# Optimization experiments

Hardware: AMD Instinct MI355X
Metric: run time of the kernel (lower is better)

The kernel has to match this reference:

```python
import jax, jax.numpy as jnp
import numpy as np

N, T, F_IN, HID, LAT, E = 20000, 16, 65, 128, 64, 320000
F = F_IN - 1


def setup_inputs() -> dict:
    key = jax.random.key(0)
    ks = jax.random.split(key, 10)
    def w(k, shape, fan):
        return jax.random.normal(k, shape, jnp.float32) / np.sqrt(fan).astype(np.float32)
    return dict(
        x=jax.random.normal(ks[0], (N, T, F_IN), jnp.float32),
        enc_W=w(ks[1], (F, HID), F), enc_b=jnp.zeros((HID,), jnp.float32),
        enc_ln_g=jnp.ones((HID,), jnp.float32), enc_ln_b=jnp.zeros((HID,), jnp.float32),
        lstm1_Wih=w(ks[2], (HID, 4 * LAT), HID), lstm1_Whh=w(ks[3], (LAT, 4 * LAT), LAT),
        lstm1_b=jnp.zeros((4 * LAT,), jnp.float32),
        lstm2_Wih=w(ks[4], (LAT, 4 * HID), LAT), lstm2_Whh=w(ks[5], (HID, 4 * HID), HID),
        lstm2_b=jnp.zeros((4 * HID,), jnp.float32),
        dec_ln_g=jnp.ones((HID,), jnp.float32), dec_ln_b=jnp.zeros((HID,), jnp.float32),
        dec_W=w(ks[6], (HID, F), HID), dec_b=jnp.zeros((F,), jnp.float32),
        edge_index=jax.random.randint(ks[7], (2, E), 0, N, dtype=jnp.int64),
    )


def _ln(x, g, b):
    m = x.mean(-1, keepdims=True)
    v = x.var(-1, keepdims=True)
    return (x - m) * jax.lax.rsqrt(v + 1e-5) * g + b


def _gcn(xs, W, b, src, dst, dinv):
    # xs: (T, N, Fin); PyG GCNConv: sym-normalized A+I, then linear. Linear first (same math).
    n = xs.shape[1]
    xw = jnp.einsum('tnf,fh->tnh', xs, W)
    norm = (dinv[src] * dinv[dst])[:, None]  # (E,1)
    def body(_, xt):  # scatter one frame at a time to bound (E,H) intermediate
        return None, jax.ops.segment_sum(xt[src] * norm, dst, num_segments=n)
    _, agg = jax.lax.scan(body, None, xw)
    # self-loop term: norm_ii = dinv_i^2
    return agg + (dinv ** 2)[None, :, None] * xw + b


def _lstm(x_seq, Wih, Whh, b):
    # x_seq: (S, B, in) -> outputs (S, B, H); PyTorch gate order i,f,g,o
    H = Whh.shape[0]
    B = x_seq.shape[1]
    def step(carry, xt):
        h, c = carry
        gates = xt @ Wih + h @ Whh + b
        i, f, g, o = jnp.split(gates, 4, axis=-1)
        c = jax.nn.sigmoid(f) * c + jax.nn.sigmoid(i) * jnp.tanh(g)
        h = jax.nn.sigmoid(o) * jnp.tanh(c)
        return (h, c), h
    z0 = jnp.zeros((B, H), x_seq.dtype)
    _, hs = jax.lax.scan(step, (z0, z0), x_seq)
    return hs


def reference(x, enc_W, enc_b, enc_ln_g, enc_ln_b,
              lstm1_Wih, lstm1_Whh, lstm1_b,
              lstm2_Wih, lstm2_Whh, lstm2_b,
              dec_ln_g, dec_ln_b, dec_W, dec_b, edge_index):
    src, dst = edge_index[0], edge_index[1]
    deg = jax.ops.segment_sum(jnp.ones(src.shape[0], x.dtype), dst,
                              num_segments=x.shape[0]) + 1.0  # +1 for self loop
    dinv = jax.lax.rsqrt(deg)
    importance = x[:, :, -1:]                      # (N,T,1)
    xs = (x[:, :, :-1] * importance).transpose(1, 0, 2)   # frame-major (T,N,F)
    h = _ln(_gcn(xs, enc_W, enc_b, src, dst, dinv), enc_ln_g, enc_ln_b)  # (T,N,HID)
    # temporal encoder: batch=N nodes, sequence over T frames
    z = _lstm(h, lstm1_Wih, lstm1_Whh, lstm1_b)    # (T,N,LAT)
    z_nt = z.transpose(1, 0, 2)                    # (N,T,LAT)
    # temporal decoder: original code feeds (1, N, LAT) per frame -> sequence over
    # NODES with fresh state each frame; batch the T independent frames together.
    hd = _lstm(z_nt, lstm2_Wih, lstm2_Whh, lstm2_b)  # scan over nodes -> (N,T,HID)
    hd = _ln(hd.transpose(1, 0, 2), dec_ln_g, dec_ln_b)  # (T,N,HID)
    rec = _gcn(hd, dec_W, dec_b, src, dst, dinv).transpose(1, 0, 2)  # (N,T,F)
    reconstructed = jnp.concatenate([rec, importance], axis=2)        # (N,T,F_IN)
    return z_nt, reconstructed
```

## Files before the change

### kernel.cpp

```cpp
#include <hip/hip_runtime.h>
#include <hip/hip_fp16.h>
#include <stdint.h>

#define N_NODES 20000
#define T_STEPS 16
#define F_INPUT 65
#define F_DIM   64
#define HID     128
#define LAT     64
#define N_EDGES 320000

#define WARMUP  32

typedef _Float16 f16x8 __attribute__((ext_vector_type(8)));
typedef float f32x4 __attribute__((ext_vector_type(4)));

__device__ __forceinline__ float rcp_fast(float x){ return __builtin_amdgcn_rcpf(x); }
__device__ __forceinline__ float sigm(float x){ return rcp_fast(1.0f + __expf(-x)); }
__device__ __forceinline__ float tanh_fast(float x){
  float e = __expf(2.0f * x);
  return 1.0f - 2.0f * rcp_fast(e + 1.0f);
}

__global__ void k_zero(int* deg){
  int i = blockIdx.x * 256 + threadIdx.x;
  if (i < N_NODES) deg[i] = 0;
}

__global__ void k_count(const int* __restrict__ ei, int* __restrict__ deg){
  int e = blockIdx.x * 256 + threadIdx.x;
  if (e < N_EDGES) atomicAdd(&deg[ei[N_EDGES + e]], 1);
}

__global__ void k_scan(const int* __restrict__ deg, int* __restrict__ offs,
                       float* __restrict__ dinv, int* __restrict__ cursor){
  __shared__ int sbuf[1024];
  __shared__ int carry;
  int tid = threadIdx.x;
  if (tid == 0){ carry = 0; offs[0] = 0; }
  __syncthreads();
  for (int base = 0; base < N_NODES; base += 1024){
    int cb = carry;
    int v = (base + tid < N_NODES) ? deg[base + tid] : 0;
    sbuf[tid] = v;
    __syncthreads();
    for (int off = 1; off < 1024; off <<= 1){
      int add = (tid >= off) ? sbuf[tid - off] : 0;
      __syncthreads();
      sbuf[tid] += add;
      __syncthreads();
    }
    if (base + tid < N_NODES){
      offs[base + tid + 1] = cb + sbuf[tid];
      cursor[base + tid] = cb + sbuf[tid] - v;
      dinv[base + tid] = rsqrtf((float)v + 1.0f);
    }
    __syncthreads();
    if (tid == 1023) carry = cb + sbuf[1023];
    __syncthreads();
  }
}

__global__ void k_fill(const int* __restrict__ ei, const float* __restrict__ dinv,
                       int* __restrict__ cursor, int* __restrict__ csrc,
                       float* __restrict__ cw){
  int e = blockIdx.x * 256 + threadIdx.x;
  if (e < N_EDGES){
    int s = ei[e], d = ei[N_EDGES + e];
    int p = atomicAdd(&cursor[d], 1);
    csrc[p] = s;
    cw[p] = dinv[s] * dinv[d];
  }
}

__global__ void k_xsw(const float* __restrict__ x, __half* __restrict__ xsw){
  int idx = blockIdx.x * 256 + threadIdx.x;
  if (idx < N_NODES * T_STEPS * F_DIM){
    int nt = idx >> 6;
    int k = idx & 63;
    float imp = x[(size_t)nt * F_INPUT + F_DIM];
    xsw[idx] = __float2half(x[(size_t)nt * F_INPUT + k] * imp);
  }
}

__device__ __forceinline__ void acc_row(uint2 rv, float wv,
                                        float& a0, float& a1, float& a2, float& a3){
  __half2 h01 = __builtin_bit_cast(__half2, rv.x);
  __half2 h23 = __builtin_bit_cast(__half2, rv.y);
  a0 += wv * __half2float(h01.x); a1 += wv * __half2float(h01.y);
  a2 += wv * __half2float(h23.x); a3 += wv * __half2float(h23.y);
}

__global__ void k_wprep(const float* __restrict__ W1ih, const float* __restrict__ W1hh,
                        const float* __restrict__ Wih2, const float* __restrict__ Whh2,
                        const float* __restrict__ encW, const float* __restrict__ decW,
                        __half* __restrict__ WB1, __half* __restrict__ WZ2,
                        __half* __restrict__ WB2, __half* __restrict__ WBe,
                        __half* __restrict__ WBd){
  int idx = blockIdx.x * 256 + threadIdx.x;
  if (idx < 49152){
    int j = idx & 7;
    int lane = (idx >> 3) & 63;
    int tk = idx >> 9;
    int kt = tk % 6;
    int T = tk / 6;
    int k = 32 * kt + 8 * (lane >> 4) + j;
    int col = 16 * T + (lane & 15);
    float v = (k < 128) ? W1ih[k * 256 + col] : W1hh[(k - 128) * 256 + col];
    WB1[idx] = __float2half(v);
  } else if (idx < 81920){
    int i2 = idx - 49152;
    int j = i2 & 7;
    int lane = (i2 >> 3) & 63;
    int fid = i2 >> 9;
    int kt = fid & 1;
    int T = fid >> 1;
    int k = 32 * kt + 8 * (lane >> 4) + j;
    int col = 16 * T + (lane & 15);
    WZ2[i2] = __float2half(Wih2[k * 512 + col]);
  } else if (idx < 147456){
    int i2 = idx - 81920;
    int j = i2 & 7;
    int lane = (i2 >> 3) & 63;
    int kt = (i2 >> 9) & 3;
    int T = i2 >> 11;
    int k = 32 * kt + 8 * (lane >> 4) + j;
    int col = T * 16 + (lane & 15);
    WB2[i2] = __float2half(Whh2[k * 512 + col]);
  } else if (idx < 155648){
    int i2 = idx - 147456;
    int j = i2 & 7;
    int lane = (i2 >> 3) & 63;
    int fid = i2 >> 9;
    int kt = fid & 1;
    int T = fid >> 1;
    int k = 32 * kt + 8 * (lane >> 4) + j;
    int col = 16 * T + (lane & 15);
    WBe[i2] = __float2half(encW[k * 128 + col]);
  } else if (idx < 163840){
    int i2 = idx - 155648;
    int j = i2 & 7;
    int lane = (i2 >> 3) & 63;
    int fid = i2 >> 9;
    int kt = fid & 3;
    int T = fid >> 2;
    int k = 32 * kt + 8 * (lane >> 4) + j;
    int col = 16 * T + (lane & 15);
    WBd[i2] = __float2half(decW[k * 64 + col]);
  }
}

__global__ __launch_bounds__(256) void k_enc(
    const __half* __restrict__ xsw, const int* __restrict__ offs,
    const int* __restrict__ csrc, const float* __restrict__ cw,
    const float* __restrict__ dinv, const __half* __restrict__ WBe,
    const float* __restrict__ encb, const float* __restrict__ lng,
    const float* __restrict__ lnb, __half* __restrict__ henc){
  __shared__ __align__(16) char ush[16 * 160];
  __shared__ float hb[16 * 132];
  const int tid = threadIdx.x;
  const int w = tid >> 6, lane = tid & 63;
  const int qf = lane & 15, gf = lane >> 4;
  const int t = tid >> 4, q = tid & 15;
  const f32x4 z4 = {0.f, 0.f, 0.f, 0.f};

  f16x8 wbe[2][2];
  float eb[2];
  {
    const f16x8* Bp = (const f16x8*)WBe;
    #pragma unroll
    for (int tt = 0; tt < 2; ++tt){
      #pragma unroll
      for (int kt = 0; kt < 2; ++kt)
        wbe[tt][kt] = Bp[((2 * w + tt) * 2 + kt) * 64 + lane];
      eb[tt] = encb[16 * (2 * w + tt) + qf];
    }
  }

  for (int nn = 0; nn < 4; ++nn){
    int n = blockIdx.x * 4 + nn;
    __syncthreads();
    float a0 = 0.f, a1 = 0.f, a2 = 0.f, a3 = 0.f;
    int beg = offs[n], end = offs[n + 1];
    int e = beg;
    for (; e + 8 <= end; e += 8){
      int sx[8]; float wx[8]; uint2 rx[8];
      #pragma unroll
      for (int k = 0; k < 8; ++k){ sx[k] = csrc[e + k]; wx[k] = cw[e + k]; }
      #pragma unroll
      for (int k = 0; k < 8; ++k)
        rx[k] = *reinterpret_cast<const uint2*>(&xsw[((size_t)(sx[k] * 16 + t)) * 64 + 4 * q]);
      #pragma unroll
      for (int k = 0; k < 8; ++k) acc_row(rx[k], wx[k], a0, a1, a2, a3);
    }
    for (; e < end; ++e){
      int s = csrc[e];
      float wv = cw[e];
      uint2 rv = *reinterpret_cast<const uint2*>(&xsw[((size_t)(s * 16 + t)) * 64 + 4 * q]);
      acc_row(rv, wv, a0, a1, a2, a3);
    }
    float di = dinv[n];
    float d2 = di * di;
    {
      uint2 rv = *reinterpret_cast<const uint2*>(&xsw[((size_t)(n * 16 + t)) * 64 + 4 * q]);
      acc_row(rv, d2, a0, a1, a2, a3);
    }
    {
      __half2 p01 = __floats2half2_rn(a0, a1);
      __half2 p23 = __floats2half2_rn(a2, a3);
      uint2 pk;
      pk.x = __builtin_bit_cast(uint32_t, p01);
      pk.y = __builtin_bit_cast(uint32_t, p23);
      *(uint2*)(ush + t * 160 + 8 * q) = pk;
    }
    __syncthreads();
    {
      f16x8 A0 = *(const f16x8*)(ush + qf * 160 + 16 * gf);
      f16x8 A1 = *(const f16x8*)(ush + qf * 160 + 64 + 16 * gf);
      #pragma unroll
      for (int tt = 0; tt < 2; ++tt){
        f32x4 acc = __builtin_amdgcn_mfma_f32_16x16x32_f16(A0, wbe[tt][0], z4, 0, 0, 0);
        acc = __builtin_amdgcn_mfma_f32_16x16x32_f16(A1, wbe[tt][1], acc, 0, 0, 0);
        #pragma unroll
        for (int r = 0; r < 4; ++r)
          hb[(4 * gf + r) * 132 + 16 * (2 * w + tt) + qf] = acc[r] + eb[tt];
      }
    }
    __syncthreads();
    {
      float v[8];
      float s1 = 0.f, s2 = 0.f;
      #pragma unroll
      for (int r = 0; r < 8; ++r){
        v[r] = hb[t * 132 + q + 16 * r];
        s1 += v[r]; s2 += v[r] * v[r];
      }
      #pragma unroll
      for (int m = 1; m < 16; m <<= 1){
        s1 += __shfl_xor(s1, m, 16);
        s2 += __shfl_xor(s2, m, 16);
      }
      float mean = s1 * (1.0f / 128.0f);
      float var = s2 * (1.0f / 128.0f) - mean * mean;
      float rstd = rsqrtf(var + 1e-5f);
      #pragma unroll
      for (int r = 0; r < 8; ++r){
        int j = q + 16 * r;
        henc[((size_t)t * N_NODES + n) * 128 + j] =
            __float2half((v[r] - mean) * rstd * lng[j] + lnb[j]);
      }
    }
  }
}

__global__ __launch_bounds__(256) void k_l1mm(
    const __half* __restrict__ henc, const __half* __restrict__ WB1,
    const float* __restrict__ b1, float* __restrict__ out0,
    __half* __restrict__ zh){
  __shared__ __align__(16) char xt[16 * 272];
  __shared__ __align__(16) char hs[2][16 * 144];
  const int tid = threadIdx.x;
  const int w = tid >> 6, lane = tid & 63;
  const int q = lane & 15, g = lane >> 4;
  const int n0 = blockIdx.x * 16;
  const int u = 16 * w + q;
  const f32x4 z4 = {0.f, 0.f, 0.f, 0.f};

  f16x8 wb[4][6];
  {
    const f16x8* WBp = (const f16x8*)WB1;
    #pragma unroll
    for (int gate = 0; gate < 4; ++gate){
      #pragma unroll
      for (int kt = 0; kt < 6; ++kt){
        wb[gate][kt] = WBp[((4 * gate + w) * 6 + kt) * 64 + lane];
      }
    }
  }
  float bi = b1[u], bf = b1[64 + u], bg = b1[128 + u], bo = b1[192 + u];

  for (int i = tid; i < 576; i += 256) *(int*)(hs[0] + 4 * i) = 0;
  float creg[4] = {0.f, 0.f, 0.f, 0.f};
  const int sni = tid >> 4, sk0 = (tid & 15) * 8;
  const __half* hsrc0 = henc + ((size_t)(n0 + sni) * 128 + sk0);

  #pragma unroll 1
  for (int t = 0; t < T_STEPS; ++t){
    __syncthreads();
    *(f16x8*)(xt + sni * 272 + 2 * sk0) = *(const f16x8*)(hsrc0 + (size_t)t * N_NODES * 128);
    __syncthreads();
    const char* hrow = hs[t & 1] + q * 144 + 16 * g;
    f16x8 a0 = *(const f16x8*)(xt + 272 * q + 16 * g);
    f16x8 a1 = *(const f16x8*)(xt + 272 * q + 64 + 16 * g);
    f16x8 a2 = *(const f16x8*)(xt + 272 * q + 128 + 16 * g);
    f16x8 a3 = *(const f16x8*)(xt + 272 * q + 192 + 16 * g);
    f16x8 a4 = *(const f16x8*)(hrow);
    f16x8 a5 = *(const f16x8*)(hrow + 64);
    f32x4 ai = z4, af = z4, ag = z4, ao = z4;
#define MF(A, B, C) __builtin_amdgcn_mfma_f32_16x16x32_f16((A), (B), (C), 0, 0, 0)
    ai = MF(a0, wb[0][0], ai); af = MF(a0, wb[1][0], af);
    ag = MF(a0, wb[2][0], ag); ao = MF(a0, wb[3][0], ao);
    ai = MF(a1, wb[0][1], ai); af = MF(a1, wb[1][1], af);
    ag = MF(a1, wb[2][1], ag); ao = MF(a1, wb[3][1], ao);
    ai = MF(a2, wb[0][2], ai); af = MF(a2, wb[1][2], af);
    ag = MF(a2, wb[2][2], ag); ao = MF(a2, wb[3][2], ao);
    ai = MF(a3, wb[0][3], ai); af = MF(a3, wb[1][3], af);
    ag = MF(a3, wb[2][3], ag); ao = MF(a3, wb[3][3], ao);
    ai = MF(a4, wb[0][4], ai); af = MF(a4, wb[1][4], af);
    ag = MF(a4, wb[2][4], ag); ao = MF(a4, wb[3][4], ao);
    ai = MF(a5, wb[0][5], ai); af = MF(a5, wb[1][5], af);
    ag = MF(a5, wb[2][5], ag); ao = MF(a5, wb[3][5], ao);
#undef MF
    #pragma unroll
    for (int r = 0; r < 4; ++r){
      int node = 4 * g + r;
      float gi = ai[r] + bi, gf = af[r] + bf;
      float gg = ag[r] + bg, go = ao[r] + bo;
      float c = sigm(gf) * creg[r] + sigm(gi) * tanh_fast(gg);
      creg[r] = c;
      float h = sigm(go) * tanh_fast(c);
      _Float16 hh = (_Float16)h;
      *(_Float16*)(hs[(t + 1) & 1] + node * 144 + 2 * u) = hh;
      size_t oidx = ((size_t)(n0 + node) * 16 + t) * 64 + u;
      out0[oidx] = h;
      zh[oidx] = __builtin_bit_cast(__half, hh);
    }
  }
}

__global__ __launch_bounds__(512) void k_lstm2(
    const __half* __restrict__ zh, const __half* __restrict__ WB2,
    const __half* __restrict__ WZ2, const float* __restrict__ b2,
    __half* __restrict__ hd){
  __shared__ __align__(16) char hls[2][16 * 288];
  const int tid = threadIdx.x;
  const int w = tid >> 6;
  const int lane = tid & 63;
  const int q = lane & 15;
  const int g = lane >> 4;
  const int s = blockIdx.x;
  const int u = 16 * w + q;
  const int n0 = 78 * s + (s < 32 ? s : 32);
  const int n1 = n0 + (s < 32 ? 79 : 78);
  const int n_start = (s == 0) ? 0 : (n0 - WARMUP);
  const f32x4 zz4 = {0.f, 0.f, 0.f, 0.f};

  f16x8 wb[4][4];
  f16x8 wz[4][2];
  {
    const f16x8* WBp = (const f16x8*)WB2;
    const f16x8* WZp = (const f16x8*)WZ2;
    #pragma unroll
    for (int gate = 0; gate < 4; ++gate){
      #pragma unroll
      for (int kt = 0; kt < 4; ++kt)
        wb[gate][kt] = WBp[((gate * 8 + w) * 4 + kt) * 64 + lane];
      #pragma unroll
      for (int kt = 0; kt < 2; ++kt)
        wz[gate][kt] = WZp[((gate * 8 + w) * 2 + kt) * 64 + lane];
    }
  }
  const float b_i = b2[128 * 0 + u];
  const float b_f = b2[128 * 1 + u];
  const float b_g = b2[128 * 2 + u];
  const float b_o = b2[128 * 3 + u];

  for (int i = tid; i < 2304; i += 512) ((int*)hls)[i] = 0;

  int rdoff[4];
  #pragma unroll
  for (int kt = 0; kt < 4; ++kt)
    rdoff[kt] = q * 288 + 64 * kt + 16 * g;

  const __half* zq = zh + 64 * q + 8 * g;
  f16x8 za0k0, za0k1, za1k0, za1k1, za2k0, za2k1, za3k0, za3k1;
#define LDZ(K0, K1, NN)                                                        \
  { const __half* p_ = zq + (size_t)(NN) * 1024;                               \
    K0 = *(const f16x8*)(p_); K1 = *(const f16x8*)(p_ + 32); }
  LDZ(za0k0, za0k1, n_start + 0)
  LDZ(za1k0, za1k1, n_start + 1)
  LDZ(za2k0, za2k1, n_start + 2)
  LDZ(za3k0, za3k1, n_start + 3)

  float creg[4] = {0.f, 0.f, 0.f, 0.f};
  __half* hdp = hd + u;
  __syncthreads();

#define MFM(A, B, C) __builtin_amdgcn_mfma_f32_16x16x32_f16((A), (B), (C), 0, 0, 0)
#define L2_CORE(CUR, ZK0, ZK1, DO_STORE, NN)                                   \
  {                                                                            \
    const char* rb = hls[CUR];                                                 \
    f16x8 a0 = *(const f16x8*)(rb + rdoff[0]);                                 \
    f16x8 a1 = *(const f16x8*)(rb + rdoff[1]);                                 \
    f16x8 a2 = *(const f16x8*)(rb + rdoff[2]);                                 \
    f16x8 a3 = *(const f16x8*)(rb + rdoff[3]);                                 \
    f32x4 acc[4];                                                              \
    _Pragma("unroll")                                                          \
    for (int gate = 0; gate < 4; ++gate){                                      \
      acc[gate] = MFM(ZK0, wz[gate][0], zz4);                                  \
      acc[gate] = MFM(ZK1, wz[gate][1], acc[gate]);                            \
    }                                                                          \
    _Pragma("unroll")                                                          \
    for (int gate = 0; gate < 4; ++gate) acc[gate] = MFM(a0, wb[gate][0], acc[gate]); \
    _Pragma("unroll")                                                          \
    for (int gate = 0; gate < 4; ++gate) acc[gate] = MFM(a1, wb[gate][1], acc[gate]); \
    _Pragma("unroll")                                                          \
    for (int gate = 0; gate < 4; ++gate) acc[gate] = MFM(a2, wb[gate][2], acc[gate]); \
    _Pragma("unroll")                                                          \
    for (int gate = 0; gate < 4; ++gate) acc[gate] = MFM(a3, wb[gate][3], acc[gate]); \
    _Pragma("unroll")                                                          \
    for (int r = 0; r < 4; ++r){                                               \
      float gi = acc[0][r] + b_i;                                              \
      float gf = acc[1][r] + b_f;                                              \
      float gg = acc[2][r] + b_g;                                              \
      float go = acc[3][r] + b_o;                                              \
      float ei = __expf(-gi), ef = __expf(-gf);                                \
      float eg = __expf(2.f * gg), eo = __expf(-go);                           \
      float pi1 = 1.f + ei, pf1 = 1.f + ef, pg1 = eg + 1.f;                    \
      float pig_ = pi1 * pg1;                                                  \
      float num = creg[r] * pig_ + (eg - 1.f) * pf1;                           \
      float c = num * rcp_fast(pf1 * pig_);                                    \
      creg[r] = c;                                                             \
      float ec = __expf(2.f * c);                                              \
      float h = (ec - 1.f) * rcp_fast((1.f + eo) * (ec + 1.f));                \
      *(_Float16*)(hls[CUR ^ 1] + (4 * g + r) * 288 + 2 * u) = (_Float16)h;    \
      if (DO_STORE && (NN) < n1)                                               \
        hdp[(size_t)(NN) * 2048 + (4 * g + r) * 128] = __float2half(h);        \
    }                                                                          \
    __builtin_amdgcn_sched_barrier(0);                                         \
    asm volatile("s_waitcnt lgkmcnt(0)" ::: "memory");                         \
    __builtin_amdgcn_s_barrier();                                              \
    __builtin_amdgcn_sched_barrier(0);                                         \
  }

  #pragma unroll 1
  for (int n = n_start; n < n0; n += 4){
    L2_CORE(0, za0k0, za0k1, 0, n)     LDZ(za0k0, za0k1, n + 4)
    L2_CORE(1, za1k0, za1k1, 0, n)     LDZ(za1k0, za1k1, n + 5)
    L2_CORE(0, za2k0, za2k1, 0, n)     LDZ(za2k0, za2k1, n + 6)
    L2_CORE(1, za3k0, za3k1, 0, n)     LDZ(za3k0, za3k1, n + 7)
  }
  #pragma unroll 1
  for (int n = n0; n < n1; n += 4){
    L2_CORE(0, za0k0, za0k1, 1, n + 0) LDZ(za0k0, za0k1, n + 4)
    L2_CORE(1, za1k0, za1k1, 1, n + 1) LDZ(za1k0, za1k1, n + 5)
    L2_CORE(0, za2k0, za2k1, 1, n + 2) LDZ(za2k0, za2k1, n + 6)
    L2_CORE(1, za3k0, za3k1, 1, n + 3) LDZ(za3k0, za3k1, n + 7)
  }
#undef L2_CORE
#undef MFM
#undef LDZ
}

__global__ __launch_bounds__(256) void k_decproj(
    const __half* __restrict__ hd, const __half* __restrict__ WBd,
    const float* __restrict__ lng, const float* __restrict__ lnb,
    __half* __restrict__ y){
  __shared__ float xr[16 * 132];
  __shared__ __align__(16) char xrh[16 * 288];
  const int tid = threadIdx.x;
  const int w = tid >> 6, lane = tid & 63;
  const int qf = lane & 15, gf = lane >> 4;
  const int t = tid >> 4, q = tid & 15;
  const f32x4 z4 = {0.f, 0.f, 0.f, 0.f};

  f16x8 wbd[4];
  {
    const f16x8* Bp = (const f16x8*)WBd;
    #pragma unroll
    for (int kt = 0; kt < 4; ++kt)
      wbd[kt] = Bp[(w * 4 + kt) * 64 + lane];
  }

  for (int nn = 0; nn < 4; ++nn){
    int n = blockIdx.x * 4 + nn;
    __syncthreads();
    {
      f16x8 hv = *(const f16x8*)(hd + (size_t)n * 2048 + tid * 8);
      int tt2 = tid >> 4, k0 = (tid & 15) * 8;
      #pragma unroll
      for (int jj = 0; jj < 8; ++jj) xr[tt2 * 132 + k0 + jj] = (float)hv[jj];
    }
    __syncthreads();
    {
      float v[8];
      float s1 = 0.f, s2 = 0.f;
      #pragma unroll
      for (int r = 0; r < 8; ++r){
        v[r] = xr[t * 132 + q + 16 * r];
        s1 += v[r]; s2 += v[r] * v[r];
      }
      #pragma unroll
      for (int m = 1; m < 16; m <<= 1){
        s1 += __shfl_xor(s1, m, 16);
        s2 += __shfl_xor(s2, m, 16);
      }
      float mean = s1 * (1.0f / 128.0f);
      float var = s2 * (1.0f / 128.0f) - mean * mean;
      float rstd = rsqrtf(var + 1e-5f);
      #pragma unroll
      for (int r = 0; r < 8; ++r){
        int jj = q + 16 * r;
        *(_Float16*)(xrh + t * 288 + 2 * jj) =
            (_Float16)((v[r] - mean) * rstd * lng[jj] + lnb[jj]);
      }
    }
    __syncthreads();
    {
      f16x8 A0 = *(const f16x8*)(xrh + qf * 288 + 16 * gf);
      f16x8 A1 = *(const f16x8*)(xrh + qf * 288 + 64 + 16 * gf);
      f16x8 A2 = *(const f16x8*)(xrh + qf * 288 + 128 + 16 * gf);
      f16x8 A3 = *(const f16x8*)(xrh + qf * 288 + 192 + 16 * gf);
      f32x4 acc = __builtin_amdgcn_mfma_f32_16x16x32_f16(A0, wbd[0], z4, 0, 0, 0);
      acc = __builtin_amdgcn_mfma_f32_16x16x32_f16(A1, wbd[1], acc, 0, 0, 0);
      acc = __builtin_amdgcn_mfma_f32_16x16x32_f16(A2, wbd[2], acc, 0, 0, 0);
      acc = __builtin_amdgcn_mfma_f32_16x16x32_f16(A3, wbd[3], acc, 0, 0, 0);
      #pragma unroll
      for (int r = 0; r < 4; ++r)
        y[((size_t)n * 16 + 4 * gf + r) * 64 + 16 * w + qf] = __float2half(acc[r]);
    }
  }
}

__global__ __launch_bounds__(256) void k_decagg(
    const __half* __restrict__ y, const int* __restrict__ offs,
    const int* __restrict__ csrc, const float* __restrict__ cw,
    const float* __restrict__ dinv, const float* __restrict__ decb,
    const float* __restrict__ x, float* __restrict__ out1){
  int n = blockIdx.x, tid = threadIdx.x;
  int t = tid >> 4, q = tid & 15;
  float a0 = 0.f, a1 = 0.f, a2 = 0.f, a3 = 0.f;
  int beg = offs[n], end = offs[n + 1];
  int e = beg;
  for (; e + 8 <= end; e += 8){
    int sx[8]; float wx[8]; uint2 rx[8];
    #pragma unroll
    for (int k = 0; k < 8; ++k){ sx[k] = csrc[e + k]; wx[k] = cw[e + k]; }
    #pragma unroll
    for (int k = 0; k < 8; ++k)
      rx[k] = *reinterpret_cast<const uint2*>(&y[((size_t)(sx[k] * 16 + t)) * 64 + 4 * q]);
    #pragma unroll
    for (int k = 0; k < 8; ++k) acc_row(rx[k], wx[k], a0, a1, a2, a3);
  }
  for (; e < end; ++e){
    int s = csrc[e];
    float wv = cw[e];
    uint2 rv = *reinterpret_cast<const uint2*>(&y[((size_t)(s * 16 + t)) * 64 + 4 * q]);
    acc_row(rv, wv, a0, a1, a2, a3);
  }
  float di = dinv[n];
  float d2 = di * di;
  {
    uint2 rv = *reinterpret_cast<const uint2*>(&y[((size_t)(n * 16 + t)) * 64 + 4 * q]);
    acc_row(rv, d2, a0, a1, a2, a3);
  }
  a0 += decb[4 * q + 0]; a1 += decb[4 * q + 1];
  a2 += decb[4 * q + 2]; a3 += decb[4 * q + 3];
  size_t ob = ((size_t)n * 16 + t) * 65;
  out1[ob + 4 * q + 0] = a0;
  out1[ob + 4 * q + 1] = a1;
  out1[ob + 4 * q + 2] = a2;
  out1[ob + 4 * q + 3] = a3;
  if (q == 0) out1[ob + 64] = x[((size_t)n * 16 + t) * 65 + 64];
}

extern "C" void kernel_launch(void* const* d_in, const int* in_sizes, int n_in,
                              void* d_out, int out_size, void* d_ws, size_t ws_size,
                              hipStream_t stream){
  (void)in_sizes; (void)n_in; (void)out_size; (void)ws_size;
  const float* x     = (const float*)d_in[0];
  const float* encW  = (const float*)d_in[1];
  const float* encb  = (const float*)d_in[2];
  const float* encg  = (const float*)d_in[3];
  const float* encbl = (const float*)d_in[4];
  const float* W1ih  = (const float*)d_in[5];
  const float* W1hh  = (const float*)d_in[6];
  const float* b1    = (const float*)d_in[7];
  const float* W2ih  = (const float*)d_in[8];
  const float* W2hh  = (const float*)d_in[9];
  const float* b2    = (const float*)d_in[10];
  const float* dlg   = (const float*)d_in[11];
  const float* dlb   = (const float*)d_in[12];
  const float* decW  = (const float*)d_in[13];
  const float* decb  = (const float*)d_in[14];
  const int*   ei    = (const int*)d_in[15];

  char* w = (char*)d_ws;
  auto alloc = [&](size_t bytes) -> char* {
    char* p = w;
    w += (bytes + 255) & ~(size_t)255;
    return p;
  };
  int*   deg    = (int*)  alloc((size_t)N_NODES * 4);
  float* dinv   = (float*)alloc((size_t)N_NODES * 4);
  int*   offs   = (int*)  alloc((size_t)(N_NODES + 1) * 4);
  int*   cursor = (int*)  alloc((size_t)N_NODES * 4);
  int*   csrc   = (int*)  alloc((size_t)N_EDGES * 4);
  float* cwt    = (float*)alloc((size_t)N_EDGES * 4);
  __half* xsw   = (__half*)alloc((size_t)N_NODES * T_STEPS * 64 * 2);
  __half* henc  = (__half*)alloc((size_t)T_STEPS * N_NODES * 128 * 2);
  __half* hd    = (__half*)alloc((size_t)N_NODES * T_STEPS * 128 * 2);
  __half* yh    = (__half*)alloc((size_t)N_NODES * T_STEPS * 64 * 2);
  __half* zh    = (__half*)alloc((size_t)N_NODES * T_STEPS * 64 * 2 + 32768);
  __half* WB1   = (__half*)alloc((size_t)49152 * 2);
  __half* WZ2   = (__half*)alloc((size_t)32768 * 2);
  __half* WB2   = (__half*)alloc((size_t)65536 * 2);
  __half* WBe   = (__half*)alloc((size_t)8192 * 2);
  __half* WBd   = (__half*)alloc((size_t)8192 * 2);

  float* out0 = (float*)d_out;
  float* out1 = out0 + (size_t)N_NODES * T_STEPS * 64;

  k_zero<<<(N_NODES + 255) / 256, 256, 0, stream>>>(deg);
  k_count<<<(N_EDGES + 255) / 256, 256, 0, stream>>>(ei, deg);
  k_scan<<<1, 1024, 0, stream>>>(deg, offs, dinv, cursor);
  k_fill<<<(N_EDGES + 255) / 256, 256, 0, stream>>>(ei, dinv, cursor, csrc, cwt);
  k_xsw<<<(N_NODES * T_STEPS * 64 + 255) / 256, 256, 0, stream>>>(x, xsw);
  k_wprep<<<640, 256, 0, stream>>>(W1ih, W1hh, W2ih, W2hh, encW, decW,
                                   WB1, WZ2, WB2, WBe, WBd);
  k_enc<<<5000, 256, 0, stream>>>(xsw, offs, csrc, cwt, dinv, WBe, encb, encg, encbl, henc);
  k_l1mm<<<1250, 256, 0, stream>>>(henc, WB1, b1, out0, zh);
  k_lstm2<<<256, 512, 0, stream>>>(zh, WB2, WZ2, b2, hd);
  k_decproj<<<5000, 256, 0, stream>>>(hd, WBd, dlg, dlb, yh);
  k_decagg<<<N_NODES, 256, 0, stream>>>(yh, offs, csrc, cwt, dinv, decb, x, out1);
}
```

Before: 544.0 us.

## Process two nodes per 512-thread block in encoder and decoder aggregation; pad LSTM2 LDS rows

```diff
diff --git a/kernel.cpp b/kernel.cpp
--- a/kernel.cpp
+++ b/kernel.cpp
@@ -150,18 +150,21 @@
   }
 }
 
-__global__ __launch_bounds__(256) void k_enc(
+__global__ __launch_bounds__(512) void k_enc(
     const __half* __restrict__ xsw, const int* __restrict__ offs,
     const int* __restrict__ csrc, const float* __restrict__ cw,
     const float* __restrict__ dinv, const __half* __restrict__ WBe,
     const float* __restrict__ encb, const float* __restrict__ lng,
     const float* __restrict__ lnb, __half* __restrict__ henc){
-  __shared__ __align__(16) char ush[16 * 160];
-  __shared__ float hb[16 * 132];
+  __shared__ __align__(16) char ush[2][16 * 160];
+  __shared__ float hb[2][16 * 132];
   const int tid = threadIdx.x;
+  const int n2 = tid >> 8;
+  const int tid8 = tid & 255;
+  const int t = tid8 >> 4, q = tid8 & 15;
   const int w = tid >> 6, lane = tid & 63;
+  const int wloc = w & 3, nw = w >> 2;
   const int qf = lane & 15, gf = lane >> 4;
-  const int t = tid >> 4, q = tid & 15;
   const f32x4 z4 = {0.f, 0.f, 0.f, 0.f};
 
   f16x8 wbe[2][2];
@@ -172,14 +175,13 @@
     for (int tt = 0; tt < 2; ++tt){
       #pragma unroll
       for (int kt = 0; kt < 2; ++kt)
-        wbe[tt][kt] = Bp[((2 * w + tt) * 2 + kt) * 64 + lane];
-      eb[tt] = encb[16 * (2 * w + tt) + qf];
-    }
-  }
-
-  for (int nn = 0; nn < 4; ++nn){
-    int n = blockIdx.x * 4 + nn;
-    __syncthreads();
+        wbe[tt][kt] = Bp[((2 * wloc + tt) * 2 + kt) * 64 + lane];
+      eb[tt] = encb[16 * (2 * wloc + tt) + qf];
+    }
+  }
+
+  const int n = blockIdx.x * 2 + n2;
+  {
     float a0 = 0.f, a1 = 0.f, a2 = 0.f, a3 = 0.f;
     int beg = offs[n], end = offs[n + 1];
     int e = beg;
@@ -205,50 +207,48 @@
       uint2 rv = *reinterpret_cast<const uint2*>(&xsw[((size_t)(n * 16 + t)) * 64 + 4 * q]);
       acc_row(rv, d2, a0, a1, a2, a3);
     }
-    {
-      __half2 p01 = __floats2half2_rn(a0, a1);
-      __half2 p23 = __floats2half2_rn(a2, a3);
-      uint2 pk;
-      pk.x = __builtin_bit_cast(uint32_t, p01);
-      pk.y = __builtin_bit_cast(uint32_t, p23);
-      *(uint2*)(ush + t * 160 + 8 * q) = pk;
-    }
-    __syncthreads();
-    {
-      f16x8 A0 = *(const f16x8*)(ush + qf * 160 + 16 * gf);
-      f16x8 A1 = *(const f16x8*)(ush + qf * 160 + 64 + 16 * gf);
-      #pragma unroll
-      for (int tt = 0; tt < 2; ++tt){
-        f32x4 acc = __builtin_amdgcn_mfma_f32_16x16x32_f16(A0, wbe[tt][0], z4, 0, 0, 0);
-        acc = __builtin_amdgcn_mfma_f32_16x16x32_f16(A1, wbe[tt][1], acc, 0, 0, 0);
-        #pragma unroll
-        for (int r = 0; r < 4; ++r)
-          hb[(4 * gf + r) * 132 + 16 * (2 * w + tt) + qf] = acc[r] + eb[tt];
-      }
-    }
-    __syncthreads();
-    {
-      float v[8];
-      float s1 = 0.f, s2 = 0.f;
-      #pragma unroll
-      for (int r = 0; r < 8; ++r){
-        v[r] = hb[t * 132 + q + 16 * r];
-        s1 += v[r]; s2 += v[r] * v[r];
-      }
-      #pragma unroll
-      for (int m = 1; m < 16; m <<= 1){
-        s1 += __shfl_xor(s1, m, 16);
-        s2 += __shfl_xor(s2, m, 16);
-      }
-      float mean = s1 * (1.0f / 128.0f);
-      float var = s2 * (1.0f / 128.0f) - mean * mean;
-      float rstd = rsqrtf(var + 1e-5f);
-      #pragma unroll
-      for (int r = 0; r < 8; ++r){
-        int j = q + 16 * r;
-        henc[((size_t)t * N_NODES + n) * 128 + j] =
-            __float2half((v[r] - mean) * rstd * lng[j] + lnb[j]);
-      }
+    __half2 p01 = __floats2half2_rn(a0, a1);
+    __half2 p23 = __floats2half2_rn(a2, a3);
+    uint2 pk;
+    pk.x = __builtin_bit_cast(uint32_t, p01);
+    pk.y = __builtin_bit_cast(uint32_t, p23);
+    *(uint2*)(ush[n2] + t * 160 + 8 * q) = pk;
+  }
+  __syncthreads();
+  {
+    f16x8 A0 = *(const f16x8*)(ush[nw] + qf * 160 + 16 * gf);
+    f16x8 A1 = *(const f16x8*)(ush[nw] + qf * 160 + 64 + 16 * gf);
+    #pragma unroll
+    for (int tt = 0; tt < 2; ++tt){
+      f32x4 acc = __builtin_amdgcn_mfma_f32_16x16x32_f16(A0, wbe[tt][0], z4, 0, 0, 0);
+      acc = __builtin_amdgcn_mfma_f32_16x16x32_f16(A1, wbe[tt][1], acc, 0, 0, 0);
+      #pragma unroll
+      for (int r = 0; r < 4; ++r)
+        hb[nw][(4 * gf + r) * 132 + 16 * (2 * wloc + tt) + qf] = acc[r] + eb[tt];
+    }
+  }
+  __syncthreads();
+  {
+    float v[8];
+    float s1 = 0.f, s2 = 0.f;
+    #pragma unroll
+    for (int r = 0; r < 8; ++r){
+      v[r] = hb[n2][t * 132 + q + 16 * r];
+      s1 += v[r]; s2 += v[r] * v[r];
+    }
+    #pragma unroll
+    for (int m = 1; m < 16; m <<= 1){
+      s1 += __shfl_xor(s1, m, 16);
+      s2 += __shfl_xor(s2, m, 16);
+    }
+    float mean = s1 * (1.0f / 128.0f);
+    float var = s2 * (1.0f / 128.0f) - mean * mean;
+    float rstd = rsqrtf(var + 1e-5f);
+    #pragma unroll
+    for (int r = 0; r < 8; ++r){
+      int j = q + 16 * r;
+      henc[((size_t)t * N_NODES + n) * 128 + j] =
+          __float2half((v[r] - mean) * rstd * lng[j] + lnb[j]);
     }
   }
 }
@@ -332,7 +332,7 @@
     const __half* __restrict__ zh, const __half* __restrict__ WB2,
     const __half* __restrict__ WZ2, const float* __restrict__ b2,
     __half* __restrict__ hd){
-  __shared__ __align__(16) char hls[2][16 * 288];
+  __shared__ __align__(16) char hls[2][16 * 304];
   const int tid = threadIdx.x;
   const int w = tid >> 6;
   const int lane = tid & 63;
@@ -365,12 +365,12 @@
   const float b_g = b2[128 * 2 + u];
   const float b_o = b2[128 * 3 + u];
 
-  for (int i = tid; i < 2304; i += 512) ((int*)hls)[i] = 0;
+  for (int i = tid; i < 2432; i += 512) ((int*)hls)[i] = 0;
 
   int rdoff[4];
   #pragma unroll
   for (int kt = 0; kt < 4; ++kt)
-    rdoff[kt] = q * 288 + 64 * kt + 16 * g;
+    rdoff[kt] = q * 304 + 64 * kt + 16 * g;
 
   const __half* zq = zh + 64 * q + 8 * g;
   f16x8 za0k0, za0k1, za1k0, za1k1, za2k0, za2k1, za3k0, za3k1;
@@ -423,7 +423,7 @@
       creg[r] = c;                                                             \
       float ec = __expf(2.f * c);                                              \
       float h = (ec - 1.f) * rcp_fast((1.f + eo) * (ec + 1.f));                \
-      *(_Float16*)(hls[CUR ^ 1] + (4 * g + r) * 288 + 2 * u) = (_Float16)h;    \
+      *(_Float16*)(hls[CUR ^ 1] + (4 * g + r) * 304 + 2 * u) = (_Float16)h;    \
       if (DO_STORE && (NN) < n1)                                               \
         hdp[(size_t)(NN) * 2048 + (4 * g + r) * 128] = __float2half(h);        \
     }                                                                          \
@@ -522,13 +522,15 @@
   }
 }
 
-__global__ __launch_bounds__(256) void k_decagg(
+__global__ __launch_bounds__(512) void k_decagg(
     const __half* __restrict__ y, const int* __restrict__ offs,
     const int* __restrict__ csrc, const float* __restrict__ cw,
     const float* __restrict__ dinv, const float* __restrict__ decb,
     const float* __restrict__ x, float* __restrict__ out1){
-  int n = blockIdx.x, tid = threadIdx.x;
-  int t = tid >> 4, q = tid & 15;
+  int tid = threadIdx.x;
+  int n = blockIdx.x * 2 + (tid >> 8);
+  int tid8 = tid & 255;
+  int t = tid8 >> 4, q = tid8 & 15;
   float a0 = 0.f, a1 = 0.f, a2 = 0.f, a3 = 0.f;
   int beg = offs[n], end = offs[n + 1];
   int e = beg;
@@ -618,9 +620,9 @@
   k_xsw<<<(N_NODES * T_STEPS * 64 + 255) / 256, 256, 0, stream>>>(x, xsw);
   k_wprep<<<640, 256, 0, stream>>>(W1ih, W1hh, W2ih, W2hh, encW, decW,
                                    WB1, WZ2, WB2, WBe, WBd);
-  k_enc<<<5000, 256, 0, stream>>>(xsw, offs, csrc, cwt, dinv, WBe, encb, encg, encbl, henc);
+  k_enc<<<N_NODES / 2, 512, 0, stream>>>(xsw, offs, csrc, cwt, dinv, WBe, encb, encg, encbl, henc);
   k_l1mm<<<1250, 256, 0, stream>>>(henc, WB1, b1, out0, zh);
   k_lstm2<<<256, 512, 0, stream>>>(zh, WB2, WZ2, b2, hd);
   k_decproj<<<5000, 256, 0, stream>>>(hd, WBd, dlg, dlb, yh);
-  k_decagg<<<N_NODES, 256, 0, stream>>>(yh, offs, csrc, cwt, dinv, decb, x, out1);
-}
+  k_decagg<<<N_NODES / 2, 512, 0, stream>>>(yh, offs, csrc, cwt, dinv, decb, x, out1);
+}
```

Measured after the change: 569.1 us. 1.05x slower.
